# Kernel tuning notes

Measured on AMD Instinct MI355X. Metric: run time of the kernel, lower is better.

The kernel has to match this reference:

```python
import jax, jax.numpy as jnp
import numpy as np

NUM_IDS = 128  # number of distinct instance ids (static segment count)
W_FG = 1.0
W_BG = 1.0
W_SIN = 1.0
W_COS = 1.0
W_CENT = 1.0


def setup_inputs() -> dict:
    key = jax.random.key(0)
    k1, k2, k3 = jax.random.split(key, 3)
    B, H, W = 16, 768, 768
    prediction = jax.random.normal(k1, (B, 2, H, W), dtype=jnp.float32)
    instances = jax.random.randint(k2, (B, H, W), 0, NUM_IDS, dtype=jnp.int32)
    labels = (instances > 0).astype(jnp.int32)  # fg where an instance exists
    centerdir_gt = jax.random.normal(k3, (B, 5, H, W), dtype=jnp.float32)
    return {"prediction": prediction, "instances": instances,
            "labels": labels, "centerdir_gt": centerdir_gt}


def _instance_weights(instances, labels):
    # Vectorized equivalent of the torch per-id Python loop normalization.
    B = instances.shape[0]
    flat = instances.reshape(B, -1)  # [B, HW]
    # counts[b, k] = #pixels in image b with instance id k
    counts = jnp.zeros((B, NUM_IDS), jnp.float32).at[
        jnp.arange(B)[:, None], flat].add(1.0)
    # total instances across the whole batch (ids > 0 present per image)
    num_instances = jnp.sum(counts[:, 1:] > 0).astype(jnp.float32)
    # total background pixels across the whole batch (id == 0)
    num_bg_pixels = jnp.sum(counts[:, 0])
    # normalization per (b, id): id==0 -> bg_total*2 ; id>0 -> count*num_inst*2
    is_bg_id = (jnp.arange(NUM_IDS) == 0)[None, :]
    norm = jnp.where(is_bg_id,
                     num_bg_pixels * 2.0,
                     jnp.maximum(counts, 1.0) * num_instances * 2.0)
    inv_norm = jnp.take_along_axis(1.0 / norm, flat, axis=1)  # [B, HW]
    inv_norm = inv_norm.reshape(instances.shape)[:, None]      # [B,1,H,W]
    base = jnp.where(labels[:, None] == 0, W_BG, W_FG).astype(jnp.float32)
    return jax.lax.stop_gradient(base * inv_norm)  # computed under no_grad


def reference(prediction, instances, labels, centerdir_gt):
    pred_sin = prediction[:, 0:1]  # [B,1,H,W]
    pred_cos = prediction[:, 1:2]
    gt_sin = centerdir_gt[:, 2:3]
    gt_cos = centerdir_gt[:, 3:4]

    mask_weights = _instance_weights(instances, labels)

    loss_sin = jnp.sum(mask_weights * jnp.abs(pred_sin - gt_sin), axis=(1, 2, 3))
    loss_cos = jnp.sum(mask_weights * jnp.abs(pred_cos - gt_cos), axis=(1, 2, 3))

    loss_sin = W_SIN * loss_sin
    loss_cos = W_COS * loss_cos
    loss_centers = W_CENT * jnp.zeros_like(loss_sin)  # localization disabled
    loss_direction_total = loss_sin + loss_cos
    loss = loss_direction_total + loss_centers

    eps = jnp.sum(prediction) * 0.0  # keeps grad graph attached, as in torch
    return (loss + eps, loss_direction_total + eps, loss_centers + eps,
            loss_sin + eps, loss_cos + eps)
```

## Files before the change

### kernel.cpp

```cpp
#include <hip/hip_runtime.h>

#define BATCH 16
#define HW (768 * 768)
#define NIDS 128
#define GROUPS (HW / 4)


__global__ __launch_bounds__(256) void hist_kernel(const int* __restrict__ inst,
                                                   unsigned int* __restrict__ counts) {
    __shared__ unsigned int lhist[NIDS];
    const int b = blockIdx.y;
    for (int i = threadIdx.x; i < NIDS; i += blockDim.x) lhist[i] = 0u;
    __syncthreads();

    const int4* src = (const int4*)(inst + (size_t)b * HW);
    for (int g = blockIdx.x * blockDim.x + threadIdx.x; g < GROUPS;
         g += gridDim.x * blockDim.x) {
        int4 v = src[g];
        atomicAdd(&lhist[v.x & 127], 1u);
        atomicAdd(&lhist[v.y & 127], 1u);
        atomicAdd(&lhist[v.z & 127], 1u);
        atomicAdd(&lhist[v.w & 127], 1u);
    }
    __syncthreads();
    for (int i = threadIdx.x; i < NIDS; i += blockDim.x)
        if (lhist[i]) atomicAdd(&counts[b * NIDS + i], lhist[i]);
}

__global__ __launch_bounds__(256) void norm_kernel(const unsigned int* __restrict__ counts,
                                                   float* __restrict__ inv_norm,
                                                   float* __restrict__ sums) {
    unsigned int ninst = 0u, nbg = 0u;
    for (int i = threadIdx.x; i < BATCH * NIDS; i += blockDim.x) {
        const unsigned int c = counts[i];
        if ((i & 127) == 0) nbg += c;
        else ninst += (c > 0u) ? 1u : 0u;
    }
    for (int off = 32; off; off >>= 1) {
        ninst += __shfl_down(ninst, off, 64);
        nbg   += __shfl_down(nbg,   off, 64);
    }
    __shared__ unsigned int s_ninst[4], s_nbg[4];
    __shared__ float s_f[2];
    const int wid = threadIdx.x >> 6, lane = threadIdx.x & 63;
    if (lane == 0) { s_ninst[wid] = ninst; s_nbg[wid] = nbg; }
    __syncthreads();
    if (threadIdx.x == 0) {
        unsigned int a = 0u, c = 0u;
        for (int i = 0; i < 4; ++i) { a += s_ninst[i]; c += s_nbg[i]; }
        s_f[0] = (float)a;
        s_f[1] = (float)c;
    }
    __syncthreads();
    const float num_instances = s_f[0];
    const float num_bg = s_f[1];
    for (int i = threadIdx.x; i < BATCH * NIDS; i += blockDim.x) {
        const float c = (float)counts[i];
        const float norm = ((i & 127) == 0) ? (num_bg * 2.0f)
                                            : (fmaxf(c, 1.0f) * num_instances * 2.0f);
        inv_norm[i] = 1.0f / norm;
    }
    if (threadIdx.x < 32) sums[threadIdx.x] = 0.0f;
}

__global__ __launch_bounds__(256) void loss_kernel(const int* __restrict__ inst,
                                                   const float* __restrict__ pred,
                                                   const float* __restrict__ gt,
                                                   const float* __restrict__ inv_norm,
                                                   float* __restrict__ sums) {
    __shared__ float tbl[NIDS];
    const int b = blockIdx.y;
    for (int i = threadIdx.x; i < NIDS; i += blockDim.x) tbl[i] = inv_norm[b * NIDS + i];
    __syncthreads();

    const int4*   ip = (const int4*)  (inst + (size_t)b * HW);
    const float4* ps = (const float4*)(pred + (size_t)b * 2 * HW);
    const float4* pc = (const float4*)(pred + (size_t)b * 2 * HW + HW);
    const float4* gs = (const float4*)(gt   + (size_t)b * 5 * HW + 2 * (size_t)HW);
    const float4* gc = (const float4*)(gt   + (size_t)b * 5 * HW + 3 * (size_t)HW);

    float acc_s = 0.0f, acc_c = 0.0f;
    for (int g = blockIdx.x * blockDim.x + threadIdx.x; g < GROUPS;
         g += gridDim.x * blockDim.x) {
        const int4   v = ip[g];
        const float4 a = ps[g];
        const float4 p = pc[g];
        const float4 c = gs[g];
        const float4 d = gc[g];
        const float w0 = tbl[v.x & 127];
        const float w1 = tbl[v.y & 127];
        const float w2 = tbl[v.z & 127];
        const float w3 = tbl[v.w & 127];
        acc_s += w0 * fabsf(a.x - c.x) + w1 * fabsf(a.y - c.y) +
                 w2 * fabsf(a.z - c.z) + w3 * fabsf(a.w - c.w);
        acc_c += w0 * fabsf(p.x - d.x) + w1 * fabsf(p.y - d.y) +
                 w2 * fabsf(p.z - d.z) + w3 * fabsf(p.w - d.w);
    }

    for (int off = 32; off; off >>= 1) {
        acc_s += __shfl_down(acc_s, off, 64);
        acc_c += __shfl_down(acc_c, off, 64);
    }
    __shared__ float s_s[4], s_c[4];
    const int wid = threadIdx.x >> 6, lane = threadIdx.x & 63;
    if (lane == 0) { s_s[wid] = acc_s; s_c[wid] = acc_c; }
    __syncthreads();
    if (threadIdx.x == 0) {
        float ts = 0.0f, tc = 0.0f;
        for (int i = 0; i < 4; ++i) { ts += s_s[i]; tc += s_c[i]; }
        atomicAdd(&sums[b], ts);
        atomicAdd(&sums[BATCH + b], tc);
    }
}

__global__ void fin_kernel(const float* __restrict__ sums, float* __restrict__ out) {
    const int b = threadIdx.x;
    if (b < BATCH) {
        const float s = sums[b];
        const float c = sums[BATCH + b];
        const float tot = s + c;
        out[b]      = tot;
        out[16 + b] = tot;
        out[32 + b] = 0.0f;
        out[48 + b] = s;
        out[64 + b] = c;
    }
}

extern "C" void kernel_launch(void* const* d_in, const int* in_sizes, int n_in,
                              void* d_out, int out_size, void* d_ws, size_t ws_size,
                              hipStream_t stream) {
    const float* prediction = (const float*)d_in[0];
    const int*   instances  = (const int*)d_in[1];
    const float* centerdir  = (const float*)d_in[3];
    float* out = (float*)d_out;

    unsigned int* counts  = (unsigned int*)d_ws;
    float* inv_norm       = (float*)((char*)d_ws + 8192);
    float* sums           = (float*)((char*)d_ws + 16384);

    hipMemsetAsync(counts, 0, BATCH * NIDS * sizeof(unsigned int), stream);

    hist_kernel<<<dim3(72, BATCH), 256, 0, stream>>>(instances, counts);
    norm_kernel<<<1, 256, 0, stream>>>(counts, inv_norm, sums);
    loss_kernel<<<dim3(144, BATCH), 256, 0, stream>>>(instances, prediction, centerdir,
                                                      inv_norm, sums);
    fin_kernel<<<1, 64, 0, stream>>>(sums, out);
}
```

Baseline: 329.0 us.

## Fuse histogram and loss into single pass with per-id partial sums

Because the weight depends only on (batch, id), the loss can be factored as sum over ids of inv_norm times the per-id sum of absolute errors. The new kernel reads instances, predictions and targets once, accumulating per-id counts and L1 sums in per-wavefront shared-memory histograms, then flushes them to global memory with atomics. A small final kernel computes the normalisation and combines the per-id sums. This removes the second read of the instance map and two kernel launches, at the cost of three shared-memory atomics per pixel (float atomics may contend) and a different float summation order.

```diff
diff --git a/kernel.cpp b/kernel.cpp
--- a/kernel.cpp
+++ b/kernel.cpp
@@ -4,35 +4,83 @@
 #define HW (768 * 768)
 #define NIDS 128
 #define GROUPS (HW / 4)
+#define NBLK 144
 
 
-__global__ __launch_bounds__(256) void hist_kernel(const int* __restrict__ inst,
-                                                   unsigned int* __restrict__ counts) {
-    __shared__ unsigned int lhist[NIDS];
+__global__ __launch_bounds__(256) void fused_kernel(const int* __restrict__ inst,
+                                                    const float* __restrict__ pred,
+                                                    const float* __restrict__ gt,
+                                                    float* __restrict__ g_sin,
+                                                    float* __restrict__ g_cos,
+                                                    unsigned int* __restrict__ g_cnt) {
+    __shared__ float        s_sin[4][NIDS];
+    __shared__ float        s_cos[4][NIDS];
+    __shared__ unsigned int s_cnt[4][NIDS];
+
     const int b = blockIdx.y;
-    for (int i = threadIdx.x; i < NIDS; i += blockDim.x) lhist[i] = 0u;
+    for (int i = threadIdx.x; i < 4 * NIDS; i += 256) {
+        s_sin[i >> 7][i & 127] = 0.0f;
+        s_cos[i >> 7][i & 127] = 0.0f;
+        s_cnt[i >> 7][i & 127] = 0u;
+    }
     __syncthreads();
 
-    const int4* src = (const int4*)(inst + (size_t)b * HW);
-    for (int g = blockIdx.x * blockDim.x + threadIdx.x; g < GROUPS;
-         g += gridDim.x * blockDim.x) {
-        int4 v = src[g];
-        atomicAdd(&lhist[v.x & 127], 1u);
-        atomicAdd(&lhist[v.y & 127], 1u);
-        atomicAdd(&lhist[v.z & 127], 1u);
-        atomicAdd(&lhist[v.w & 127], 1u);
+    const int wid = threadIdx.x >> 6;
+    const int4*   ip = (const int4*)  (inst + (size_t)b * HW);
+    const float4* ps = (const float4*)(pred + (size_t)b * 2 * HW);
+    const float4* pc = (const float4*)(pred + (size_t)b * 2 * HW + HW);
+    const float4* gs = (const float4*)(gt   + (size_t)b * 5 * HW + 2 * (size_t)HW);
+    const float4* gc = (const float4*)(gt   + (size_t)b * 5 * HW + 3 * (size_t)HW);
+
+    for (int g = blockIdx.x * 256 + threadIdx.x; g < GROUPS; g += NBLK * 256) {
+        const int4   v = ip[g];
+        const float4 a = ps[g];
+        const float4 p = pc[g];
+        const float4 c = gs[g];
+        const float4 d = gc[g];
+
+        const int i0 = v.x & 127, i1 = v.y & 127, i2 = v.z & 127, i3 = v.w & 127;
+        atomicAdd(&s_sin[wid][i0], fabsf(a.x - c.x));
+        atomicAdd(&s_cos[wid][i0], fabsf(p.x - d.x));
+        atomicAdd(&s_cnt[wid][i0], 1u);
+        atomicAdd(&s_sin[wid][i1], fabsf(a.y - c.y));
+        atomicAdd(&s_cos[wid][i1], fabsf(p.y - d.y));
+        atomicAdd(&s_cnt[wid][i1], 1u);
+        atomicAdd(&s_sin[wid][i2], fabsf(a.z - c.z));
+        atomicAdd(&s_cos[wid][i2], fabsf(p.z - d.z));
+        atomicAdd(&s_cnt[wid][i2], 1u);
+        atomicAdd(&s_sin[wid][i3], fabsf(a.w - c.w));
+        atomicAdd(&s_cos[wid][i3], fabsf(p.w - d.w));
+        atomicAdd(&s_cnt[wid][i3], 1u);
     }
     __syncthreads();
-    for (int i = threadIdx.x; i < NIDS; i += blockDim.x)
-        if (lhist[i]) atomicAdd(&counts[b * NIDS + i], lhist[i]);
+
+    if (threadIdx.x < NIDS) {
+        const int id = threadIdx.x;
+        const float fs = s_sin[0][id] + s_sin[1][id] + s_sin[2][id] + s_sin[3][id];
+        const float fc = s_cos[0][id] + s_cos[1][id] + s_cos[2][id] + s_cos[3][id];
+        const unsigned int n = s_cnt[0][id] + s_cnt[1][id] + s_cnt[2][id] + s_cnt[3][id];
+        if (n) {
+            atomicAdd(&g_sin[b * NIDS + id], fs);
+            atomicAdd(&g_cos[b * NIDS + id], fc);
+            atomicAdd(&g_cnt[b * NIDS + id], n);
+        }
+    }
 }
 
-__global__ __launch_bounds__(256) void norm_kernel(const unsigned int* __restrict__ counts,
-                                                   float* __restrict__ inv_norm,
-                                                   float* __restrict__ sums) {
+__global__ __launch_bounds__(256) void fin_kernel(const float* __restrict__ g_sin,
+                                                  const float* __restrict__ g_cos,
+                                                  const unsigned int* __restrict__ g_cnt,
+                                                  float* __restrict__ out) {
+    __shared__ float s_ls[BATCH], s_lc[BATCH];
+    __shared__ unsigned int s_ni[4], s_nb[4];
+    __shared__ float s_f[2];
+
+    if (threadIdx.x < BATCH) { s_ls[threadIdx.x] = 0.0f; s_lc[threadIdx.x] = 0.0f; }
+
     unsigned int ninst = 0u, nbg = 0u;
-    for (int i = threadIdx.x; i < BATCH * NIDS; i += blockDim.x) {
-        const unsigned int c = counts[i];
+    for (int i = threadIdx.x; i < BATCH * NIDS; i += 256) {
+        const unsigned int c = g_cnt[i];
         if ((i & 127) == 0) nbg += c;
         else ninst += (c > 0u) ? 1u : 0u;
     }
@@ -40,84 +88,34 @@
         ninst += __shfl_down(ninst, off, 64);
         nbg   += __shfl_down(nbg,   off, 64);
     }
-    __shared__ unsigned int s_ninst[4], s_nbg[4];
-    __shared__ float s_f[2];
     const int wid = threadIdx.x >> 6, lane = threadIdx.x & 63;
-    if (lane == 0) { s_ninst[wid] = ninst; s_nbg[wid] = nbg; }
+    if (lane == 0) { s_ni[wid] = ninst; s_nb[wid] = nbg; }
     __syncthreads();
     if (threadIdx.x == 0) {
         unsigned int a = 0u, c = 0u;
-        for (int i = 0; i < 4; ++i) { a += s_ninst[i]; c += s_nbg[i]; }
+        for (int i = 0; i < 4; ++i) { a += s_ni[i]; c += s_nb[i]; }
         s_f[0] = (float)a;
         s_f[1] = (float)c;
     }
     __syncthreads();
     const float num_instances = s_f[0];
     const float num_bg = s_f[1];
-    for (int i = threadIdx.x; i < BATCH * NIDS; i += blockDim.x) {
-        const float c = (float)counts[i];
-        const float norm = ((i & 127) == 0) ? (num_bg * 2.0f)
-                                            : (fmaxf(c, 1.0f) * num_instances * 2.0f);
-        inv_norm[i] = 1.0f / norm;
+
+    for (int i = threadIdx.x; i < BATCH * NIDS; i += 256) {
+        const int bb = i >> 7, id = i & 127;
+        const float c = (float)g_cnt[i];
+        const float norm = (id == 0) ? (num_bg * 2.0f)
+                                     : (fmaxf(c, 1.0f) * num_instances * 2.0f);
+        const float w = 1.0f / norm;
+        atomicAdd(&s_ls[bb], g_sin[i] * w);
+        atomicAdd(&s_lc[bb], g_cos[i] * w);
     }
-    if (threadIdx.x < 32) sums[threadIdx.x] = 0.0f;
-}
-
-__global__ __launch_bounds__(256) void loss_kernel(const int* __restrict__ inst,
-                                                   const float* __restrict__ pred,
-                                                   const float* __restrict__ gt,
-                                                   const float* __restrict__ inv_norm,
-                                                   float* __restrict__ sums) {
-    __shared__ float tbl[NIDS];
-    const int b = blockIdx.y;
-    for (int i = threadIdx.x; i < NIDS; i += blockDim.x) tbl[i] = inv_norm[b * NIDS + i];
     __syncthreads();
 
-    const int4*   ip = (const int4*)  (inst + (size_t)b * HW);
-    const float4* ps = (const float4*)(pred + (size_t)b * 2 * HW);
-    const float4* pc = (const float4*)(pred + (size_t)b * 2 * HW + HW);
-    const float4* gs = (const float4*)(gt   + (size_t)b * 5 * HW + 2 * (size_t)HW);
-    const float4* gc = (const float4*)(gt   + (size_t)b * 5 * HW + 3 * (size_t)HW);
-
-    float acc_s = 0.0f, acc_c = 0.0f;
-    for (int g = blockIdx.x * blockDim.x + threadIdx.x; g < GROUPS;
-         g += gridDim.x * blockDim.x) {
-        const int4   v = ip[g];
-        const float4 a = ps[g];
-        const float4 p = pc[g];
-        const float4 c = gs[g];
-        const float4 d = gc[g];
-        const float w0 = tbl[v.x & 127];
-        const float w1 = tbl[v.y & 127];
-        const float w2 = tbl[v.z & 127];
-        const float w3 = tbl[v.w & 127];
-        acc_s += w0 * fabsf(a.x - c.x) + w1 * fabsf(a.y - c.y) +
-                 w2 * fabsf(a.z - c.z) + w3 * fabsf(a.w - c.w);
-        acc_c += w0 * fabsf(p.x - d.x) + w1 * fabsf(p.y - d.y) +
-                 w2 * fabsf(p.z - d.z) + w3 * fabsf(p.w - d.w);
-    }
-
-    for (int off = 32; off; off >>= 1) {
-        acc_s += __shfl_down(acc_s, off, 64);
-        acc_c += __shfl_down(acc_c, off, 64);
-    }
-    __shared__ float s_s[4], s_c[4];
-    const int wid = threadIdx.x >> 6, lane = threadIdx.x & 63;
-    if (lane == 0) { s_s[wid] = acc_s; s_c[wid] = acc_c; }
-    __syncthreads();
-    if (threadIdx.x == 0) {
-        float ts = 0.0f, tc = 0.0f;
-        for (int i = 0; i < 4; ++i) { ts += s_s[i]; tc += s_c[i]; }
-        atomicAdd(&sums[b], ts);
-        atomicAdd(&sums[BATCH + b], tc);
-    }
-}
-
-__global__ void fin_kernel(const float* __restrict__ sums, float* __restrict__ out) {
-    const int b = threadIdx.x;
-    if (b < BATCH) {
-        const float s = sums[b];
-        const float c = sums[BATCH + b];
+    if (threadIdx.x < BATCH) {
+        const int b = threadIdx.x;
+        const float s = s_ls[b];
+        const float c = s_lc[b];
         const float tot = s + c;
         out[b]      = tot;
         out[16 + b] = tot;
@@ -135,15 +133,13 @@
     const float* centerdir  = (const float*)d_in[3];
     float* out = (float*)d_out;
 
-    unsigned int* counts  = (unsigned int*)d_ws;
-    float* inv_norm       = (float*)((char*)d_ws + 8192);
-    float* sums           = (float*)((char*)d_ws + 16384);
+    float*        g_sin = (float*)d_ws;
+    float*        g_cos = (float*)((char*)d_ws + 8192);
+    unsigned int* g_cnt = (unsigned int*)((char*)d_ws + 16384);
 
-    hipMemsetAsync(counts, 0, BATCH * NIDS * sizeof(unsigned int), stream);
+    hipMemsetAsync(d_ws, 0, 24576, stream);
 
-    hist_kernel<<<dim3(72, BATCH), 256, 0, stream>>>(instances, counts);
-    norm_kernel<<<1, 256, 0, stream>>>(counts, inv_norm, sums);
-    loss_kernel<<<dim3(144, BATCH), 256, 0, stream>>>(instances, prediction, centerdir,
-                                                      inv_norm, sums);
-    fin_kernel<<<1, 64, 0, stream>>>(sums, out);
+    fused_kernel<<<dim3(NBLK, BATCH), 256, 0, stream>>>(instances, prediction, centerdir,
+                                                        g_sin, g_cos, g_cnt);
+    fin_kernel<<<1, 256, 0, stream>>>(g_sin, g_cos, g_cnt, out);
 }
```

Result: slower. 369.7 us (+12.4%).

## Replace shared-atomic histogram with per-thread byte counters and unroll loss loop

Applied to the files above, without the earlier changes.

The histogram kernel now gives each thread a private 128-entry byte histogram in shared memory, then reduces them with packed 32-bit reads instead of contended shared atomics. The loss kernel uses fixed-trip unrolled loops sized exactly to the grid, plus nontemporal loads for the streamed float inputs. Zeroing of the sums buffer moves from norm_kernel into the single memset. This relies on exact divisibility of the problem size by the grid and on per-bin counts staying under 256 per thread, and it uses much more shared memory per block.

```diff
diff --git a/kernel.cpp b/kernel.cpp
--- a/kernel.cpp
+++ b/kernel.cpp
@@ -4,34 +4,61 @@
 #define HW (768 * 768)
 #define NIDS 128
 #define GROUPS (HW / 4)
+#define HBLK 72
+#define LBLK 144
+
+typedef float f4 __attribute__((ext_vector_type(4)));
 
 
 __global__ __launch_bounds__(256) void hist_kernel(const int* __restrict__ inst,
                                                    unsigned int* __restrict__ counts) {
-    __shared__ unsigned int lhist[NIDS];
+    __shared__ unsigned int cnt32[256 * 32];
+    __shared__ unsigned int tmp[8 * 128];
+    unsigned char* cnt = (unsigned char*)cnt32;
+
     const int b = blockIdx.y;
-    for (int i = threadIdx.x; i < NIDS; i += blockDim.x) lhist[i] = 0u;
+    for (int i = threadIdx.x; i < 256 * 32; i += 256) cnt32[i] = 0u;
     __syncthreads();
 
     const int4* src = (const int4*)(inst + (size_t)b * HW);
-    for (int g = blockIdx.x * blockDim.x + threadIdx.x; g < GROUPS;
-         g += gridDim.x * blockDim.x) {
-        int4 v = src[g];
-        atomicAdd(&lhist[v.x & 127], 1u);
-        atomicAdd(&lhist[v.y & 127], 1u);
-        atomicAdd(&lhist[v.z & 127], 1u);
-        atomicAdd(&lhist[v.w & 127], 1u);
+    unsigned char* my = cnt + threadIdx.x * 128;
+
+    int g = blockIdx.x * 256 + threadIdx.x;
+    #pragma unroll
+    for (int it = 0; it < 8; ++it, g += HBLK * 256) {
+        const int4 v = src[g];
+        ++my[v.x & 127];
+        ++my[v.y & 127];
+        ++my[v.z & 127];
+        ++my[v.w & 127];
     }
     __syncthreads();
-    for (int i = threadIdx.x; i < NIDS; i += blockDim.x)
-        if (lhist[i]) atomicAdd(&counts[b * NIDS + i], lhist[i]);
+
+    const int idg = threadIdx.x & 31, h = threadIdx.x >> 5;
+    unsigned s0 = 0, s1 = 0, s2 = 0, s3 = 0;
+    #pragma unroll
+    for (int r = 0; r < 32; ++r) {
+        const unsigned v = cnt32[(h * 32 + r) * 32 + idg];
+        s0 += v & 255u; s1 += (v >> 8) & 255u; s2 += (v >> 16) & 255u; s3 += v >> 24;
+    }
+    tmp[h * 128 + idg * 4 + 0] = s0;
+    tmp[h * 128 + idg * 4 + 1] = s1;
+    tmp[h * 128 + idg * 4 + 2] = s2;
+    tmp[h * 128 + idg * 4 + 3] = s3;
+    __syncthreads();
+
+    if (threadIdx.x < NIDS) {
+        unsigned t = 0;
+        #pragma unroll
+        for (int hh = 0; hh < 8; ++hh) t += tmp[hh * 128 + threadIdx.x];
+        if (t) atomicAdd(&counts[b * NIDS + threadIdx.x], t);
+    }
 }
 
 __global__ __launch_bounds__(256) void norm_kernel(const unsigned int* __restrict__ counts,
-                                                   float* __restrict__ inv_norm,
-                                                   float* __restrict__ sums) {
+                                                   float* __restrict__ inv_norm) {
     unsigned int ninst = 0u, nbg = 0u;
-    for (int i = threadIdx.x; i < BATCH * NIDS; i += blockDim.x) {
+    for (int i = threadIdx.x; i < BATCH * NIDS; i += 256) {
         const unsigned int c = counts[i];
         if ((i & 127) == 0) nbg += c;
         else ninst += (c > 0u) ? 1u : 0u;
@@ -40,27 +67,26 @@
         ninst += __shfl_down(ninst, off, 64);
         nbg   += __shfl_down(nbg,   off, 64);
     }
-    __shared__ unsigned int s_ninst[4], s_nbg[4];
+    __shared__ unsigned int s_ni[4], s_nb[4];
     __shared__ float s_f[2];
     const int wid = threadIdx.x >> 6, lane = threadIdx.x & 63;
-    if (lane == 0) { s_ninst[wid] = ninst; s_nbg[wid] = nbg; }
+    if (lane == 0) { s_ni[wid] = ninst; s_nb[wid] = nbg; }
     __syncthreads();
     if (threadIdx.x == 0) {
         unsigned int a = 0u, c = 0u;
-        for (int i = 0; i < 4; ++i) { a += s_ninst[i]; c += s_nbg[i]; }
+        for (int i = 0; i < 4; ++i) { a += s_ni[i]; c += s_nb[i]; }
         s_f[0] = (float)a;
         s_f[1] = (float)c;
     }
     __syncthreads();
     const float num_instances = s_f[0];
     const float num_bg = s_f[1];
-    for (int i = threadIdx.x; i < BATCH * NIDS; i += blockDim.x) {
+    for (int i = threadIdx.x; i < BATCH * NIDS; i += 256) {
         const float c = (float)counts[i];
         const float norm = ((i & 127) == 0) ? (num_bg * 2.0f)
                                             : (fmaxf(c, 1.0f) * num_instances * 2.0f);
         inv_norm[i] = 1.0f / norm;
     }
-    if (threadIdx.x < 32) sums[threadIdx.x] = 0.0f;
 }
 
 __global__ __launch_bounds__(256) void loss_kernel(const int* __restrict__ inst,
@@ -70,23 +96,24 @@
                                                    float* __restrict__ sums) {
     __shared__ float tbl[NIDS];
     const int b = blockIdx.y;
-    for (int i = threadIdx.x; i < NIDS; i += blockDim.x) tbl[i] = inv_norm[b * NIDS + i];
+    for (int i = threadIdx.x; i < NIDS; i += 256) tbl[i] = inv_norm[b * NIDS + i];
     __syncthreads();
 
-    const int4*   ip = (const int4*)  (inst + (size_t)b * HW);
-    const float4* ps = (const float4*)(pred + (size_t)b * 2 * HW);
-    const float4* pc = (const float4*)(pred + (size_t)b * 2 * HW + HW);
-    const float4* gs = (const float4*)(gt   + (size_t)b * 5 * HW + 2 * (size_t)HW);
-    const float4* gc = (const float4*)(gt   + (size_t)b * 5 * HW + 3 * (size_t)HW);
+    const int4* ip = (const int4*)(inst + (size_t)b * HW);
+    const f4*   ps = (const f4*)  (pred + (size_t)b * 2 * HW);
+    const f4*   pc = (const f4*)  (pred + (size_t)b * 2 * HW + HW);
+    const f4*   gs = (const f4*)  (gt   + (size_t)b * 5 * HW + 2 * (size_t)HW);
+    const f4*   gc = (const f4*)  (gt   + (size_t)b * 5 * HW + 3 * (size_t)HW);
 
     float acc_s = 0.0f, acc_c = 0.0f;
-    for (int g = blockIdx.x * blockDim.x + threadIdx.x; g < GROUPS;
-         g += gridDim.x * blockDim.x) {
-        const int4   v = ip[g];
-        const float4 a = ps[g];
-        const float4 p = pc[g];
-        const float4 c = gs[g];
-        const float4 d = gc[g];
+    int g = blockIdx.x * 256 + threadIdx.x;
+    #pragma unroll
+    for (int it = 0; it < 4; ++it, g += LBLK * 256) {
+        const int4 v = ip[g];
+        const f4 a = __builtin_nontemporal_load(ps + g);
+        const f4 p = __builtin_nontemporal_load(pc + g);
+        const f4 c = __builtin_nontemporal_load(gs + g);
+        const f4 d = __builtin_nontemporal_load(gc + g);
         const float w0 = tbl[v.x & 127];
         const float w1 = tbl[v.y & 127];
         const float w2 = tbl[v.z & 127];
@@ -135,15 +162,15 @@
     const float* centerdir  = (const float*)d_in[3];
     float* out = (float*)d_out;
 
-    unsigned int* counts  = (unsigned int*)d_ws;
-    float* inv_norm       = (float*)((char*)d_ws + 8192);
-    float* sums           = (float*)((char*)d_ws + 16384);
+    unsigned int* counts   = (unsigned int*)d_ws;
+    float*        inv_norm = (float*)((char*)d_ws + 8192);
+    float*        sums     = (float*)((char*)d_ws + 16384);
 
-    hipMemsetAsync(counts, 0, BATCH * NIDS * sizeof(unsigned int), stream);
+    hipMemsetAsync(d_ws, 0, 16512, stream);
 
-    hist_kernel<<<dim3(72, BATCH), 256, 0, stream>>>(instances, counts);
-    norm_kernel<<<1, 256, 0, stream>>>(counts, inv_norm, sums);
-    loss_kernel<<<dim3(144, BATCH), 256, 0, stream>>>(instances, prediction, centerdir,
-                                                      inv_norm, sums);
+    hist_kernel<<<dim3(HBLK, BATCH), 256, 0, stream>>>(instances, counts);
+    norm_kernel<<<1, 256, 0, stream>>>(counts, inv_norm);
+    loss_kernel<<<dim3(LBLK, BATCH), 256, 0, stream>>>(instances, prediction, centerdir,
+                                                       inv_norm, sums);
     fin_kernel<<<1, 64, 0, stream>>>(sums, out);
 }
```

After: 333.2 us. Within noise of the previous version (+1.3%).
